# Optimization experiments

Hardware: AMD Instinct MI355X
Metric: run time of the kernel (lower is better)

The kernel has to match this reference:

```python
import jax, jax.numpy as jnp
import numpy as np
import math

HID = 768
HEADS = 12
HEAD_DIM = HID // HEADS
B, L = 64, 1024


def _xavier(key, shape):
    fan_in, fan_out = shape[0], shape[1]
    lim = math.sqrt(6.0 / (fan_in + fan_out))
    return jax.random.uniform(key, shape, jnp.float32, -lim, lim)


def setup_inputs() -> dict:
    key = jax.random.key(0)
    ks = jax.random.split(key, 12)
    inp = {
        "x_img": jax.random.normal(ks[0], (B, L, HID), jnp.float32),
        "cond": jax.random.normal(ks[1], (B, HID), jnp.float32),
        # attention projections
        "wq": _xavier(ks[2], (HID, HID)), "bq": jnp.zeros((HID,), jnp.float32),
        "wk": _xavier(ks[3], (HID, HID)), "bk": jnp.zeros((HID,), jnp.float32),
        "wv": _xavier(ks[4], (HID, HID)), "bv": jnp.zeros((HID,), jnp.float32),
        "wo": _xavier(ks[5], (HID, HID)), "bo": jnp.zeros((HID,), jnp.float32),
        # adaLN: zero-initialized in the original (keep small random so grads are non-trivial? No — stay faithful: zero init is the module's init, but zero would kill modulation. Use small random for a meaningful test.)
        "w_ada": jax.random.normal(ks[6], (HID, 6 * HID), jnp.float32) * 0.02,
        "b_ada": jnp.zeros((6 * HID,), jnp.float32),
        # MLP
        "w1": _xavier(ks[7], (HID, HID)), "b1": jnp.zeros((HID,), jnp.float32),
        "w2": _xavier(ks[8], (HID, HID)), "b2": jnp.zeros((HID,), jnp.float32),
        # LayerNorm params (norm_1: default scale=1, bias init const 1; norm_2: scale init const 1, bias default 0)
        "ln1_scale": jnp.ones((HID,), jnp.float32), "ln1_bias": jnp.ones((HID,), jnp.float32),
        "ln2_scale": jnp.ones((HID,), jnp.float32), "ln2_bias": jnp.zeros((HID,), jnp.float32),
    }
    return inp


def _layernorm(x, scale, bias, eps=1e-6):
    mu = jnp.mean(x, axis=-1, keepdims=True)
    var = jnp.var(x, axis=-1, keepdims=True)
    return (x - mu) * jax.lax.rsqrt(var + eps) * scale + bias


def _modulate(x, shift, scale):
    # shift/scale: [B, H] -> broadcast over seq axis
    return x * (1.0 + scale[:, None, :]) + shift[:, None, :]


def _attention(x, wq, bq, wk, bk, wv, bv, wo, bo):
    q = x @ wq + bq
    k = x @ wk + bk
    v = x @ wv + bv
    def split(t):
        b, l, _ = t.shape
        return t.reshape(b, l, HEADS, HEAD_DIM).transpose(0, 2, 1, 3)  # b h l d
    q, k, v = split(q), split(k), split(v)
    logits = jnp.einsum("bhqd,bhkd->bhqk", q, k) / math.sqrt(HEAD_DIM)
    attn = jax.nn.softmax(logits, axis=-1)
    out = jnp.einsum("bhqk,bhkd->bhqd", attn, v)
    out = out.transpose(0, 2, 1, 3).reshape(x.shape)  # b l (h d)
    return out @ wo + bo


def reference(x_img, cond, wq, bq, wk, bk, wv, bv, wo, bo, w_ada, b_ada,
              w1, b1, w2, b2, ln1_scale, ln1_bias, ln2_scale, ln2_bias):
    c = jax.nn.silu(cond) @ w_ada + b_ada  # [B, 6H]
    shift_msa, scale_msa, gate_msa, shift_mlp, scale_mlp, gate_mlp = jnp.split(c, 6, axis=1)

    h = _modulate(_layernorm(x_img, ln1_scale, ln1_bias), shift_msa, scale_msa)
    attn_out = _attention(h, wq, bq, wk, bk, wv, bv, wo, bo)
    x = x_img + gate_msa[:, None, :] * attn_out

    h2 = _modulate(_layernorm(x, ln2_scale, ln2_bias), shift_mlp, scale_mlp)
    mlp_out = jax.nn.silu(h2 @ w1 + b1) @ w2 + b2
    x = x + gate_mlp[:, None, :] * mlp_out
    return x
```

## Files before the change

kernel.cpp:

```cpp
#include <hip/hip_runtime.h>
#include <hip/hip_bf16.h>

typedef __bf16 bf16x8 __attribute__((ext_vector_type(8)));
typedef float  f32x4  __attribute__((ext_vector_type(4)));

#define MFMA_BF16(A_, B_, C_) __builtin_amdgcn_mfma_f32_16x16x32_bf16(A_, B_, C_, 0, 0, 0)

static constexpr int    HIDC  = 768;
static constexpr int    BB    = 64;
static constexpr int    LL    = 1024;
static constexpr int    MROWS = BB * LL;
static constexpr int    NHEAD = 12;
static constexpr int    HD    = 64;
static constexpr size_t QKV1  = (size_t)BB * NHEAD * LL * HD;
static constexpr float  QSCALE = 0.1803368801111204f;
static constexpr float  THR2   = 11.5416f;

static constexpr size_t OFF_WQKVT = 0;
static constexpr size_t OFF_WOT   = OFF_WQKVT + (size_t)2304 * 768 * 2;
static constexpr size_t OFF_W1T   = OFF_WOT   + (size_t)768 * 768 * 2;
static constexpr size_t OFF_W2T   = OFF_W1T   + (size_t)768 * 768 * 2;
static constexpr size_t OFF_BQKV  = OFF_W2T   + (size_t)768 * 768 * 2;
static constexpr size_t OFF_C     = OFF_BQKV  + (size_t)2304 * 4;
static constexpr size_t OFF_H     = OFF_C     + (size_t)64 * 4608 * 4;
static constexpr size_t OFF_AO    = OFF_H     + (size_t)MROWS * HIDC * 2;
static constexpr size_t OFF_QKV   = OFF_AO    + (size_t)MROWS * HIDC * 2;

__device__ __forceinline__ void async16(const __bf16* g, __bf16* l) {
    __builtin_amdgcn_global_load_lds((const __attribute__((address_space(1))) void*)g,
                                     (__attribute__((address_space(3))) void*)l, 16, 0, 0);
}

#define PH_BARRIER() do { __builtin_amdgcn_sched_barrier(0); asm volatile("" ::: "memory"); \
    __builtin_amdgcn_s_barrier(); asm volatile("" ::: "memory"); __builtin_amdgcn_sched_barrier(0); } while (0)

__global__ __launch_bounds__(256) void tcvt6_k(const float* __restrict__ s0, const float* __restrict__ s1,
                                               const float* __restrict__ s2, const float* __restrict__ s3,
                                               const float* __restrict__ s4, const float* __restrict__ s5,
                                               __bf16* __restrict__ dbase) {
    const int widx = blockIdx.x / 2304;
    const int i = (blockIdx.x % 2304) * 256 + threadIdx.x;
    const float* src = (widx == 0) ? s0 : (widx == 1) ? s1 : (widx == 2) ? s2
                     : (widx == 3) ? s3 : (widx == 4) ? s4 : s5;
    int kk = i / 768, n = i - kk * 768;
    dbase[(size_t)widx * 768 * 768 + (size_t)n * 768 + kk] = (__bf16)src[i];
}

__global__ __launch_bounds__(256) void bcat_k(const float* __restrict__ bq, const float* __restrict__ bk,
                                              const float* __restrict__ bv, float* __restrict__ bqkv) {
    int i = blockIdx.x * 256 + threadIdx.x;
    if (i < 2304) {
        int w = i / 768, r = i - w * 768;
        const float* p = (w == 0) ? bq : (w == 1) ? bk : bv;
        bqkv[i] = p[r];
    }
}

__global__ __launch_bounds__(256) void ada_k(const float* __restrict__ cond, const float* __restrict__ w_ada,
                                             const float* __restrict__ b_ada, float* __restrict__ c) {
    __shared__ float s[8][768];
    const int tid = threadIdx.x;
    const int bt = blockIdx.x / 18;
    const int nt = blockIdx.x % 18;
    #pragma unroll
    for (int i = 0; i < 24; ++i) {
        int idx = i * 256 + tid;
        int bb = idx / 768, kk = idx - bb * 768;
        float v = cond[(size_t)(bt * 8 + bb) * 768 + kk];
        s[bb][kk] = v / (1.f + __expf(-v));
    }
    __syncthreads();
    const int n = nt * 256 + tid;
    float acc[8];
    #pragma unroll
    for (int j = 0; j < 8; ++j) acc[j] = 0.f;
    for (int k = 0; k < 768; ++k) {
        float w = w_ada[(size_t)k * 4608 + n];
        #pragma unroll
        for (int j = 0; j < 8; ++j) acc[j] += s[j][k] * w;
    }
    float bias = b_ada[n];
    #pragma unroll
    for (int j = 0; j < 8; ++j) c[(size_t)(bt * 8 + j) * 4608 + n] = acc[j] + bias;
}

__global__ __launch_bounds__(256) void ln_mod_k(const float* __restrict__ x,
                                                const float* __restrict__ lns, const float* __restrict__ lnb,
                                                const float* __restrict__ c, int shift_off, int scale_off,
                                                __bf16* __restrict__ out) {
    const int row = blockIdx.x, tid = threadIdx.x;
    const size_t base = (size_t)row * HIDC;
    const int b = row >> 10;
    float v0 = x[base + tid], v1 = x[base + 256 + tid], v2 = x[base + 512 + tid];
    float s = v0 + v1 + v2;
    float ss = v0 * v0 + v1 * v1 + v2 * v2;
    #pragma unroll
    for (int off = 1; off < 64; off <<= 1) { s += __shfl_xor(s, off); ss += __shfl_xor(ss, off); }
    __shared__ float red[8];
    const int wave = tid >> 6, lane = tid & 63;
    if (lane == 0) { red[wave] = s; red[4 + wave] = ss; }
    __syncthreads();
    s  = red[0] + red[1] + red[2] + red[3];
    ss = red[4] + red[5] + red[6] + red[7];
    const float mu   = s * (1.f / 768.f);
    const float var  = ss * (1.f / 768.f) - mu * mu;
    const float rstd = rsqrtf(var + 1e-6f);
    const float* cb = c + (size_t)b * 4608;
    #pragma unroll
    for (int i = 0; i < 3; ++i) {
        int col = i * 256 + tid;
        float v = (i == 0) ? v0 : (i == 1) ? v1 : v2;
        float val = (v - mu) * rstd * lns[col] + lnb[col];
        val = val * (1.f + cb[scale_off + col]) + cb[shift_off + col];
        out[base + col] = (__bf16)val;
    }
}

template<int EPI>
__global__ __launch_bounds__(512, 2) void gemm256_k(const __bf16* __restrict__ A, const __bf16* __restrict__ BT,
                                                    const float* __restrict__ bias, int NBLK,
                                                    const float* __restrict__ e_res, const float* __restrict__ e_gate,
                                                    void* __restrict__ out0) {
    constexpr int K = 768;
    constexpr int NKT = K / 64;
    __shared__ __attribute__((aligned(16))) unsigned char LDSB[131072];
    const int tid = threadIdx.x;
    const int nwg = gridDim.x;
    const int cpx = nwg >> 3;
    const int bid = blockIdx.x;
    const int swz = (bid & 7) * cpx + (bid >> 3);
    const int mb = swz / NBLK, nb = swz - mb * NBLK;
    const size_t m0 = (size_t)mb * 256;
    const int n0 = nb * 256;
    const int wave = tid >> 6, lane = tid & 63;
    const int wm = wave >> 2, wn = wave & 3;
    const int lr = lane & 15, lg = lane >> 4;

    int prow[2], pcol[2], pphys[2];
    #pragma unroll
    for (int i = 0; i < 2; ++i) {
        int p = (i * 512 + tid) * 16;
        int Lb = p ^ (((p >> 9) & 1) << 5);
        prow[i] = Lb >> 7;
        pcol[i] = (Lb & 127) >> 1;
        pphys[i] = p;
    }
    auto STAGE = [&](const __bf16* gbase, size_t rowstart, int kt, int regoff) {
        #pragma unroll
        for (int i = 0; i < 2; ++i) {
            const __bf16* g = gbase + (rowstart + (size_t)prow[i]) * K + kt * 64 + pcol[i];
            async16(g, (__bf16*)(LDSB + regoff + pphys[i]));
        }
    };
    auto AFRAG = [&](int db, int mf, int ks) -> bf16x8 {
        int Lb = (mf * 16 + lr) * 128 + ks * 64 + lg * 16;
        int ph = Lb ^ (((Lb >> 9) & 1) << 5);
        return *(const bf16x8*)(LDSB + db * 65536 + wm * 16384 + ph);
    };
    auto BFRAG = [&](int db, int nf, int ks) -> bf16x8 {
        int Lb = ((wn & 1) * 64 + nf * 16 + lr) * 128 + ks * 64 + lg * 16;
        int ph = Lb ^ (((Lb >> 9) & 1) << 5);
        return *(const bf16x8*)(LDSB + db * 65536 + 32768 + (wn >> 1) * 16384 + ph);
    };

    f32x4 acc[8][4];
    #pragma unroll
    for (int i = 0; i < 8; ++i)
        #pragma unroll
        for (int j = 0; j < 4; ++j) acc[i][j] = (f32x4){0.f, 0.f, 0.f, 0.f};
    bf16x8 Af[4][2], Bf[4][2];

    STAGE(BT, (size_t)n0,       0, 32768);
    STAGE(BT, (size_t)n0 + 128, 0, 49152);
    STAGE(A,  m0,               0, 0);
    STAGE(A,  m0 + 128,         0, 16384);
    STAGE(BT, (size_t)n0,       1, 65536 + 32768);
    STAGE(BT, (size_t)n0 + 128, 1, 65536 + 49152);
    asm volatile("s_waitcnt vmcnt(4)" ::: "memory");
    PH_BARRIER();

    #pragma unroll 2
    for (int g = 0; g < NKT; ++g) {
        const int db = g & 1, dbn = db ^ 1;
        if (g + 1 < NKT) STAGE(A, m0, g + 1, dbn * 65536);
        #pragma unroll
        for (int mf = 0; mf < 4; ++mf) { Af[mf][0] = AFRAG(db, mf, 0); Af[mf][1] = AFRAG(db, mf, 1); }
        #pragma unroll
        for (int nf = 0; nf < 2; ++nf) { Bf[nf][0] = BFRAG(db, nf, 0); Bf[nf][1] = BFRAG(db, nf, 1); }
        __builtin_amdgcn_s_setprio(1);
        #pragma unroll
        for (int ks = 0; ks < 2; ++ks)
            #pragma unroll
            for (int mf = 0; mf < 4; ++mf)
                #pragma unroll
                for (int nf = 0; nf < 2; ++nf)
                    acc[mf][nf] = MFMA_BF16(Af[mf][ks], Bf[nf][ks], acc[mf][nf]);
        __builtin_amdgcn_s_setprio(0);
        PH_BARRIER();
        if (g + 1 < NKT) STAGE(A, m0 + 128, g + 1, dbn * 65536 + 16384);
        #pragma unroll
        for (int nf = 2; nf < 4; ++nf) { Bf[nf][0] = BFRAG(db, nf, 0); Bf[nf][1] = BFRAG(db, nf, 1); }
        __builtin_amdgcn_s_setprio(1);
        #pragma unroll
        for (int ks = 0; ks < 2; ++ks)
            #pragma unroll
            for (int mf = 0; mf < 4; ++mf)
                #pragma unroll
                for (int nf = 2; nf < 4; ++nf)
                    acc[mf][nf] = MFMA_BF16(Af[mf][ks], Bf[nf][ks], acc[mf][nf]);
        __builtin_amdgcn_s_setprio(0);
        PH_BARRIER();
        if (g + 2 < NKT) STAGE(BT, (size_t)n0, g + 2, db * 65536 + 32768);
        #pragma unroll
        for (int mf = 0; mf < 4; ++mf) { Af[mf][0] = AFRAG(db, mf + 4, 0); Af[mf][1] = AFRAG(db, mf + 4, 1); }
        __builtin_amdgcn_s_setprio(1);
        #pragma unroll
        for (int ks = 0; ks < 2; ++ks)
            #pragma unroll
            for (int mf = 0; mf < 4; ++mf)
                #pragma unroll
                for (int nf = 0; nf < 2; ++nf)
                    acc[mf + 4][nf] = MFMA_BF16(Af[mf][ks], Bf[nf][ks], acc[mf + 4][nf]);
        __builtin_amdgcn_s_setprio(0);
        PH_BARRIER();
        if (g + 2 < NKT) STAGE(BT, (size_t)n0 + 128, g + 2, db * 65536 + 49152);
        __builtin_amdgcn_s_setprio(1);
        #pragma unroll
        for (int ks = 0; ks < 2; ++ks)
            #pragma unroll
            for (int mf = 0; mf < 4; ++mf)
                #pragma unroll
                for (int nf = 2; nf < 4; ++nf)
                    acc[mf + 4][nf] = MFMA_BF16(Af[mf][ks], Bf[nf][ks], acc[mf + 4][nf]);
        __builtin_amdgcn_s_setprio(0);
        if (g < NKT - 2)       asm volatile("s_waitcnt vmcnt(4)" ::: "memory");
        else if (g == NKT - 2) asm volatile("s_waitcnt vmcnt(0)" ::: "memory");
        if (g + 1 < NKT) PH_BARRIER();
    }

    #pragma unroll
    for (int mf = 0; mf < 8; ++mf) {
        #pragma unroll
        for (int nf = 0; nf < 4; ++nf) {
            #pragma unroll
            for (int r = 0; r < 4; ++r) {
                const int row = wm * 128 + mf * 16 + lg * 4 + r;
                const int col = wn * 64 + nf * 16 + lr;
                const size_t m = m0 + row;
                const int n = n0 + col;
                float val = acc[mf][nf][r] + bias[n];
                if constexpr (EPI == 0) {
                    int which = n / 768, rem = n - which * 768;
                    int hh = rem >> 6, dd = rem & 63;
                    size_t bI = m >> 10, lI = m & 1023;
                    if (which == 0) {
                        ((__bf16*)out0)[(((size_t)bI * NHEAD + hh) * LL + lI) * HD + dd] = (__bf16)(val * QSCALE);
                    } else if (which == 1) {
                        ((__bf16*)out0)[QKV1 + (((size_t)bI * NHEAD + hh) * LL + lI) * HD + dd] = (__bf16)val;
                    } else {
                        int tile = (int)(lI >> 6), kv = (int)(lI & 63);
                        int ks = kv >> 5, r5 = kv & 31;
                        int lgj = (r5 >> 2) & 3;
                        int j = (r5 & 3) + ((r5 >> 4) << 2);
                        int of = dd >> 4, lr2 = dd & 15;
                        ((__bf16*)out0)[2 * QKV1 + ((size_t)bI * NHEAD + hh) * (LL * HD) + (size_t)tile * 4096
                                        + ((ks * 4 + of) * 64 + lgj * 16 + lr2) * 8 + j] = (__bf16)val;
                    }
                } else if constexpr (EPI == 1) {
                    size_t bI = m >> 10;
                    float gg = e_gate[bI * 4608 + n];
                    ((float*)out0)[m * HIDC + n] = e_res[m * HIDC + n] + gg * val;
                } else {
                    float sv = val / (1.f + __expf(-val));
                    ((__bf16*)out0)[m * HIDC + n] = (__bf16)sv;
                }
            }
        }
    }
}

__global__ __launch_bounds__(256, 4) void attn_k(const __bf16* __restrict__ qb, const __bf16* __restrict__ kb,
                                                 const __bf16* __restrict__ v2g, __bf16* __restrict__ out) {
    __shared__ __attribute__((aligned(16))) unsigned char LDSA[32768];
    const int nwg = gridDim.x;
    const int cpx = nwg >> 3;
    const int bid = blockIdx.x;
    const int swz = (bid & 7) * cpx + (bid >> 3);
    const int bh = swz >> 3;
    const int qt = swz & 7;
    const int b = bh / NHEAD, h = bh - b * NHEAD;
    const int tid = threadIdx.x;
    const int wave = tid >> 6, lane = tid & 63;
    const int lr = lane & 15, lg = lane >> 4;
    const size_t base = (size_t)bh * LL * HD;

    const int q0 = qt * 128 + wave * 32;
    bf16x8 qf[2][2];
    #pragma unroll
    for (int qi = 0; qi < 2; ++qi) {
        const __bf16* qrow = qb + base + (size_t)(q0 + qi * 16 + lr) * HD;
        qf[qi][0] = *(const bf16x8*)(qrow + lg * 8);
        qf[qi][1] = *(const bf16x8*)(qrow + 32 + lg * 8);
    }
    __builtin_amdgcn_sched_barrier(0);

    int krow[2], kcol[2];
    #pragma unroll
    for (int i = 0; i < 2; ++i) {
        int p = (i * 256 + tid) * 16;
        krow[i] = p >> 7;
        kcol[i] = (p & 127) ^ ((krow[i] & 7) << 4);
    }
    auto STAGE = [&](int t) {
        unsigned char* Lb = LDSA + (t & 1) * 16384;
        const int kv0 = t * 64;
        #pragma unroll
        for (int i = 0; i < 2; ++i) {
            const __bf16* g = kb + base + (size_t)(kv0 + krow[i]) * HD + (kcol[i] >> 1);
            async16(g, (__bf16*)(Lb + (i * 256 + tid) * 16));
        }
        #pragma unroll
        for (int i = 0; i < 2; ++i) {
            int p = (i * 256 + tid) * 16;
            const __bf16* g = v2g + base + (size_t)t * 4096 + (p >> 1);
            async16(g, (__bf16*)(Lb + 8192 + p));
        }
    };

    f32x4 acc[2][4];
    #pragma unroll
    for (int qi = 0; qi < 2; ++qi)
        #pragma unroll
        for (int i = 0; i < 4; ++i) acc[qi][i] = (f32x4){0.f, 0.f, 0.f, 0.f};
    float m_run[2] = {-1e30f, -1e30f}, l_run[2] = {0.f, 0.f};

    STAGE(0);

    for (int t = 0; t < LL / 64; ++t) {
        asm volatile("s_waitcnt vmcnt(0)" ::: "memory");
        PH_BARRIER();
        if (t + 1 < LL / 64) STAGE(t + 1);
        const unsigned char* KB = LDSA + (t & 1) * 16384;
        const unsigned char* VB = KB + 8192;

        f32x4 s[2][4];
        #pragma unroll
        for (int sf = 0; sf < 4; ++sf) {
            const int row = sf * 16 + lr;
            const bf16x8 kf0 = *(const bf16x8*)(KB + row * 128 + ((lg * 16) ^ ((row & 7) << 4)));
            const bf16x8 kf1 = *(const bf16x8*)(KB + row * 128 + ((64 + lg * 16) ^ ((row & 7) << 4)));
            #pragma unroll
            for (int qi = 0; qi < 2; ++qi) {
                f32x4 tt = (f32x4){0.f, 0.f, 0.f, 0.f};
                tt = MFMA_BF16(kf0, qf[qi][0], tt);
                tt = MFMA_BF16(kf1, qf[qi][1], tt);
                s[qi][sf] = tt;
            }
        }
        float tm[2];
        #pragma unroll
        for (int qi = 0; qi < 2; ++qi) {
            float v = -1e30f;
            #pragma unroll
            for (int sf = 0; sf < 4; ++sf)
                #pragma unroll
                for (int r = 0; r < 4; ++r) v = fmaxf(v, s[qi][sf][r]);
            v = fmaxf(v, __shfl_xor(v, 16));
            v = fmaxf(v, __shfl_xor(v, 32));
            tm[qi] = v;
        }
        const int skip = __all((tm[0] - m_run[0] <= THR2) && (tm[1] - m_run[1] <= THR2));
        if (!skip) {
            #pragma unroll
            for (int qi = 0; qi < 2; ++qi) {
                const float mnew = fmaxf(m_run[qi], tm[qi]);
                const float corr = exp2f(m_run[qi] - mnew);
                l_run[qi] *= corr;
                #pragma unroll
                for (int of = 0; of < 4; ++of)
                    #pragma unroll
                    for (int r = 0; r < 4; ++r) acc[qi][of][r] *= corr;
                m_run[qi] = mnew;
            }
        }
        #pragma unroll
        for (int qi = 0; qi < 2; ++qi) {
            float rs = 0.f;
            #pragma unroll
            for (int sf = 0; sf < 4; ++sf)
                #pragma unroll
                for (int r = 0; r < 4; ++r) { float e = exp2f(s[qi][sf][r] - m_run[qi]); s[qi][sf][r] = e; rs += e; }
            rs += __shfl_xor(rs, 16);
            rs += __shfl_xor(rs, 32);
            l_run[qi] += rs;
        }
        #pragma unroll
        for (int ks = 0; ks < 2; ++ks) {
            bf16x8 pb[2];
            #pragma unroll
            for (int qi = 0; qi < 2; ++qi)
                #pragma unroll
                for (int j = 0; j < 4; ++j) {
                    pb[qi][j]     = (__bf16)s[qi][2 * ks][j];
                    pb[qi][4 + j] = (__bf16)s[qi][2 * ks + 1][j];
                }
            #pragma unroll
            for (int of = 0; of < 4; ++of) {
                const bf16x8 vf = *(const bf16x8*)(VB + ((ks * 4 + of) * 64 + lane) * 16);
                #pragma unroll
                for (int qi = 0; qi < 2; ++qi)
                    acc[qi][of] = MFMA_BF16(vf, pb[qi], acc[qi][of]);
            }
        }
    }
    #pragma unroll
    for (int qi = 0; qi < 2; ++qi) {
        const float inv = 1.f / l_run[qi];
        const int qq = q0 + qi * 16 + lr;
        #pragma unroll
        for (int of = 0; of < 4; ++of)
            #pragma unroll
            for (int r = 0; r < 4; ++r) {
                const int d = of * 16 + lg * 4 + r;
                out[((size_t)b * LL + qq) * HIDC + h * HD + d] = (__bf16)(acc[qi][of][r] * inv);
            }
    }
}

extern "C" void kernel_launch(void* const* d_in, const int* in_sizes, int n_in,
                              void* d_out, int out_size, void* d_ws, size_t ws_size,
                              hipStream_t stream) {
    const float* x_img = (const float*)d_in[0];
    const float* cond  = (const float*)d_in[1];
    const float* wq    = (const float*)d_in[2];
    const float* bq    = (const float*)d_in[3];
    const float* wk    = (const float*)d_in[4];
    const float* bk    = (const float*)d_in[5];
    const float* wv    = (const float*)d_in[6];
    const float* bv    = (const float*)d_in[7];
    const float* wo    = (const float*)d_in[8];
    const float* bo    = (const float*)d_in[9];
    const float* w_ada = (const float*)d_in[10];
    const float* b_ada = (const float*)d_in[11];
    const float* w1    = (const float*)d_in[12];
    const float* b1    = (const float*)d_in[13];
    const float* w2    = (const float*)d_in[14];
    const float* b2    = (const float*)d_in[15];
    const float* ln1s  = (const float*)d_in[16];
    const float* ln1b  = (const float*)d_in[17];
    const float* ln2s  = (const float*)d_in[18];
    const float* ln2b  = (const float*)d_in[19];

    char* ws = (char*)d_ws;
    __bf16* wqkvT = (__bf16*)(ws + OFF_WQKVT);
    __bf16* woT   = (__bf16*)(ws + OFF_WOT);
    __bf16* w1T   = (__bf16*)(ws + OFF_W1T);
    __bf16* w2T   = (__bf16*)(ws + OFF_W2T);
    float*  bqkv  = (float*)(ws + OFF_BQKV);
    float*  cbuf  = (float*)(ws + OFF_C);
    __bf16* hbuf  = (__bf16*)(ws + OFF_H);
    __bf16* aobuf = (__bf16*)(ws + OFF_AO);
    __bf16* qkv   = (__bf16*)(ws + OFF_QKV);
    float*  xbuf  = (float*)(ws + OFF_QKV);

    dim3 blk(256);
    dim3 blk512(512);

    tcvt6_k<<<6 * 2304, blk, 0, stream>>>(wq, wk, wv, wo, w1, w2, wqkvT);
    bcat_k<<<9, blk, 0, stream>>>(bq, bk, bv, bqkv);
    ada_k<<<144, blk, 0, stream>>>(cond, w_ada, b_ada, cbuf);

    ln_mod_k<<<MROWS, blk, 0, stream>>>(x_img, ln1s, ln1b, cbuf, 0, 768, hbuf);

    gemm256_k<0><<<2304, blk512, 0, stream>>>(hbuf, wqkvT, bqkv, 9, nullptr, nullptr, (void*)qkv);

    attn_k<<<BB * NHEAD * 8, blk, 0, stream>>>(qkv, qkv + QKV1, qkv + 2 * QKV1, aobuf);

    gemm256_k<1><<<768, blk512, 0, stream>>>(aobuf, woT, bo, 3, x_img, cbuf + 2 * 768, (void*)xbuf);

    ln_mod_k<<<MROWS, blk, 0, stream>>>(xbuf, ln2s, ln2b, cbuf, 3 * 768, 4 * 768, hbuf);

    gemm256_k<2><<<768, blk512, 0, stream>>>(hbuf, w1T, b1, 3, nullptr, nullptr, (void*)aobuf);

    gemm256_k<1><<<768, blk512, 0, stream>>>(aobuf, w2T, b2, 3, xbuf, cbuf + 5 * 768, d_out);

    (void)in_sizes; (void)n_in; (void)out_size; (void)ws_size;
}
```

Measured before the change: 1.322 ms.

## Tile weight transpose through LDS and reorder GEMM fragment loads around barriers

The weight transpose/convert kernel now stages 64x64 tiles through shared memory. Reads are coalesced float4 loads and writes are 16-byte bf16x8 stores, replacing scattered per-element transposed writes. In the GEMM main loop, LDS fragment reads are issued before the next global-to-LDS stage, with extra barriers and explicit lgkmcnt waits so fragment reads overlap the async loads. Sched_barrier fences are removed, leaving the compiler freer to schedule, though the extra barriers per k-step add synchronisation cost.

After: 1.580 ms. 19.5% more time.

```diff
diff --git a/kernel.cpp b/kernel.cpp
--- a/kernel.cpp
+++ b/kernel.cpp
@@ -31,19 +31,38 @@
                                      (__attribute__((address_space(3))) void*)l, 16, 0, 0);
 }
 
-#define PH_BARRIER() do { __builtin_amdgcn_sched_barrier(0); asm volatile("" ::: "memory"); \
-    __builtin_amdgcn_s_barrier(); asm volatile("" ::: "memory"); __builtin_amdgcn_sched_barrier(0); } while (0)
+#define SYNC() do { asm volatile("" ::: "memory"); __builtin_amdgcn_s_barrier(); \
+                    asm volatile("" ::: "memory"); } while (0)
 
 __global__ __launch_bounds__(256) void tcvt6_k(const float* __restrict__ s0, const float* __restrict__ s1,
                                                const float* __restrict__ s2, const float* __restrict__ s3,
                                                const float* __restrict__ s4, const float* __restrict__ s5,
                                                __bf16* __restrict__ dbase) {
-    const int widx = blockIdx.x / 2304;
-    const int i = (blockIdx.x % 2304) * 256 + threadIdx.x;
+    __shared__ float t[64][65];
+    const int bid = blockIdx.x;
+    const int widx = bid / 144;
+    const int tb = bid - widx * 144;
+    const int kt = tb / 12, nt = tb - kt * 12;
     const float* src = (widx == 0) ? s0 : (widx == 1) ? s1 : (widx == 2) ? s2
                      : (widx == 3) ? s3 : (widx == 4) ? s4 : s5;
-    int kk = i / 768, n = i - kk * 768;
-    dbase[(size_t)widx * 768 * 768 + (size_t)n * 768 + kk] = (__bf16)src[i];
+    const int tid = threadIdx.x;
+    const int r = tid >> 4, c4 = (tid & 15) * 4;
+    #pragma unroll
+    for (int i = 0; i < 4; ++i) {
+        const float4 v = *(const float4*)(src + (size_t)(kt * 64 + r + 16 * i) * 768 + nt * 64 + c4);
+        t[r + 16 * i][c4 + 0] = v.x; t[r + 16 * i][c4 + 1] = v.y;
+        t[r + 16 * i][c4 + 2] = v.z; t[r + 16 * i][c4 + 3] = v.w;
+    }
+    __syncthreads();
+    const int n = tid >> 2, kg = (tid & 3) * 8;
+    #pragma unroll
+    for (int i = 0; i < 2; ++i) {
+        const int k = kg + i * 32;
+        bf16x8 o;
+        #pragma unroll
+        for (int j = 0; j < 8; ++j) o[j] = (__bf16)t[k + j][n];
+        *(bf16x8*)(dbase + (size_t)widx * 768 * 768 + (size_t)(nt * 64 + n) * 768 + kt * 64 + k) = o;
+    }
 }
 
 __global__ __launch_bounds__(256) void bcat_k(const float* __restrict__ bq, const float* __restrict__ bk,
@@ -177,16 +196,19 @@
     STAGE(BT, (size_t)n0,       1, 65536 + 32768);
     STAGE(BT, (size_t)n0 + 128, 1, 65536 + 49152);
     asm volatile("s_waitcnt vmcnt(4)" ::: "memory");
-    PH_BARRIER();
+    SYNC();
 
     #pragma unroll 2
     for (int g = 0; g < NKT; ++g) {
         const int db = g & 1, dbn = db ^ 1;
+        #pragma unroll
+        for (int mf = 0; mf < 4; ++mf) { Af[mf][0] = AFRAG(db, mf, 0); Af[mf][1] = AFRAG(db, mf, 1); }
+        #pragma unroll
+        for (int nf = 0; nf < 2; ++nf) { Bf[nf][0] = BFRAG(db, nf, 0); Bf[nf][1] = BFRAG(db, nf, 1); }
         if (g + 1 < NKT) STAGE(A, m0, g + 1, dbn * 65536);
-        #pragma unroll
-        for (int mf = 0; mf < 4; ++mf) { Af[mf][0] = AFRAG(db, mf, 0); Af[mf][1] = AFRAG(db, mf, 1); }
-        #pragma unroll
-        for (int nf = 0; nf < 2; ++nf) { Bf[nf][0] = BFRAG(db, nf, 0); Bf[nf][1] = BFRAG(db, nf, 1); }
+        asm volatile("s_waitcnt lgkmcnt(8)" ::: "memory");
+        SYNC();
+        asm volatile("s_waitcnt lgkmcnt(0)" ::: "memory");
         __builtin_amdgcn_s_setprio(1);
         #pragma unroll
         for (int ks = 0; ks < 2; ++ks)
@@ -196,10 +218,12 @@
                 for (int nf = 0; nf < 2; ++nf)
                     acc[mf][nf] = MFMA_BF16(Af[mf][ks], Bf[nf][ks], acc[mf][nf]);
         __builtin_amdgcn_s_setprio(0);
-        PH_BARRIER();
+        SYNC();
+        #pragma unroll
+        for (int nf = 2; nf < 4; ++nf) { Bf[nf][0] = BFRAG(db, nf, 0); Bf[nf][1] = BFRAG(db, nf, 1); }
         if (g + 1 < NKT) STAGE(A, m0 + 128, g + 1, dbn * 65536 + 16384);
-        #pragma unroll
-        for (int nf = 2; nf < 4; ++nf) { Bf[nf][0] = BFRAG(db, nf, 0); Bf[nf][1] = BFRAG(db, nf, 1); }
+        SYNC();
+        asm volatile("s_waitcnt lgkmcnt(0)" ::: "memory");
         __builtin_amdgcn_s_setprio(1);
         #pragma unroll
         for (int ks = 0; ks < 2; ++ks)
@@ -209,10 +233,12 @@
                 for (int nf = 2; nf < 4; ++nf)
                     acc[mf][nf] = MFMA_BF16(Af[mf][ks], Bf[nf][ks], acc[mf][nf]);
         __builtin_amdgcn_s_setprio(0);
-        PH_BARRIER();
+        SYNC();
+        #pragma unroll
+        for (int mf = 0; mf < 4; ++mf) { Af[mf][0] = AFRAG(db, mf + 4, 0); Af[mf][1] = AFRAG(db, mf + 4, 1); }
         if (g + 2 < NKT) STAGE(BT, (size_t)n0, g + 2, db * 65536 + 32768);
-        #pragma unroll
-        for (int mf = 0; mf < 4; ++mf) { Af[mf][0] = AFRAG(db, mf + 4, 0); Af[mf][1] = AFRAG(db, mf + 4, 1); }
+        SYNC();
+        asm volatile("s_waitcnt lgkmcnt(0)" ::: "memory");
         __builtin_amdgcn_s_setprio(1);
         #pragma unroll
         for (int ks = 0; ks < 2; ++ks)
@@ -222,7 +248,7 @@
                 for (int nf = 0; nf < 2; ++nf)
                     acc[mf + 4][nf] = MFMA_BF16(Af[mf][ks], Bf[nf][ks], acc[mf + 4][nf]);
         __builtin_amdgcn_s_setprio(0);
-        PH_BARRIER();
+        SYNC();
         if (g + 2 < NKT) STAGE(BT, (size_t)n0 + 128, g + 2, db * 65536 + 49152);
         __builtin_amdgcn_s_setprio(1);
         #pragma unroll
@@ -235,7 +261,7 @@
         __builtin_amdgcn_s_setprio(0);
         if (g < NKT - 2)       asm volatile("s_waitcnt vmcnt(4)" ::: "memory");
         else if (g == NKT - 2) asm volatile("s_waitcnt vmcnt(0)" ::: "memory");
-        if (g + 1 < NKT) PH_BARRIER();
+        if (g + 1 < NKT) SYNC();
     }
 
     #pragma unroll
@@ -302,7 +328,6 @@
         qf[qi][0] = *(const bf16x8*)(qrow + lg * 8);
         qf[qi][1] = *(const bf16x8*)(qrow + 32 + lg * 8);
     }
-    __builtin_amdgcn_sched_barrier(0);
 
     int krow[2], kcol[2];
     #pragma unroll
@@ -338,7 +363,7 @@
 
     for (int t = 0; t < LL / 64; ++t) {
         asm volatile("s_waitcnt vmcnt(0)" ::: "memory");
-        PH_BARRIER();
+        SYNC();
         if (t + 1 < LL / 64) STAGE(t + 1);
         const unsigned char* KB = LDSA + (t & 1) * 16384;
         const unsigned char* VB = KB + 8192;
@@ -466,7 +491,7 @@
     dim3 blk(256);
     dim3 blk512(512);
 
-    tcvt6_k<<<6 * 2304, blk, 0, stream>>>(wq, wk, wv, wo, w1, w2, wqkvT);
+    tcvt6_k<<<6 * 144, blk, 0, stream>>>(wq, wk, wv, wo, w1, w2, wqkvT);
     bcat_k<<<9, blk, 0, stream>>>(bq, bk, bv, bqkv);
     ada_k<<<144, blk, 0, stream>>>(cond, w_ada, b_ada, cbuf);
 
```
